# Optimization experiments

Measured on AMD Instinct MI355X. Metric: run time of the kernel, lower is better.

The kernel has to match this reference:

```python
import jax, jax.numpy as jnp
import numpy as np

B, N, E = 4, 1024, 8192
NF_IN, NF_H, NF_OUT = 32, 128, 3


def _lin(key, fan_in, fan_out):
    k1, k2 = jax.random.split(key)
    bound = 1.0 / np.sqrt(fan_in)
    W = jax.random.uniform(k1, (fan_in, fan_out), jnp.float32, -bound, bound)
    b = jax.random.uniform(k2, (fan_out,), jnp.float32, -bound, bound)
    return W, b


def setup_inputs() -> dict:
    key = jax.random.key(0)
    ks = jax.random.split(key, 16)
    x = jax.random.normal(ks[0], (B, N, NF_IN), jnp.float32)
    # One-hot receiver/sender relation matrices [B, E, N]
    recv = jax.random.randint(ks[1], (B, E), 0, N)
    send = jax.random.randint(ks[2], (B, E), 0, N)
    Rr = jax.nn.one_hot(recv, N, dtype=jnp.float32)
    Rs = jax.nn.one_hot(send, N, dtype=jnp.float32)
    neW0, neb0 = _lin(ks[3], NF_IN, NF_H)
    neW1, neb1 = _lin(ks[4], NF_H, NF_H)
    neW2, neb2 = _lin(ks[5], NF_H, NF_H)
    eeW0, eeb0 = _lin(ks[6], NF_IN * 2, NF_H)
    eeW1, eeb1 = _lin(ks[7], NF_H, NF_H)
    eeW2, eeb2 = _lin(ks[8], NF_H, NF_H)
    npW, npb = _lin(ks[9], NF_H * 2, NF_H)
    epW, epb = _lin(ks[10], NF_H * 3, NF_H)
    ppW0, ppb0 = _lin(ks[11], NF_H * 2, NF_H)
    ppW1, ppb1 = _lin(ks[12], NF_H, NF_H)
    ppW2, ppb2 = _lin(ks[13], NF_H, NF_OUT)
    return dict(x=x, Rr=Rr, Rs=Rs, pstep=2,
                neW0=neW0, neb0=neb0, neW1=neW1, neb1=neb1, neW2=neW2, neb2=neb2,
                eeW0=eeW0, eeb0=eeb0, eeW1=eeW1, eeb1=eeb1, eeW2=eeW2, eeb2=eeb2,
                npW=npW, npb=npb, epW=epW, epb=epb,
                ppW0=ppW0, ppb0=ppb0, ppW1=ppW1, ppb1=ppb1, ppW2=ppW2, ppb2=ppb2)


def _encoder(x, W0, b0, W1, b1, W2, b2):
    # Linear->ReLU x3 (ReLU after last layer too)
    h = jax.nn.relu(x @ W0 + b0)
    h = jax.nn.relu(h @ W1 + b1)
    return jax.nn.relu(h @ W2 + b2)


def _predictor(x, W0, b0, W1, b1, W2, b2):
    h = jax.nn.relu(x @ W0 + b0)
    h = jax.nn.relu(h @ W1 + b1)
    return h @ W2 + b2


def reference(x, Rr, Rs, pstep,
              neW0, neb0, neW1, neb1, neW2, neb2,
              eeW0, eeb0, eeW1, eeb1, eeW2, eeb2,
              npW, npb, epW, epb,
              ppW0, ppb0, ppW1, ppb1, ppW2, ppb2):
    node_encode = _encoder(x, neW0, neb0, neW1, neb1, neW2, neb2)  # [B,N,H]
    node_effect = node_encode
    x_r = jnp.einsum('ben,bnf->bef', Rr, x)  # gather receiver features
    x_s = jnp.einsum('ben,bnf->bef', Rs, x)  # gather sender features
    edge_encode = _encoder(jnp.concatenate([x_r, x_s], -1),
                           eeW0, eeb0, eeW1, eeb1, eeW2, eeb2)  # [B,E,H]
    for _ in range(pstep):
        ne_r = jnp.einsum('ben,bnh->beh', Rr, node_effect)
        ne_s = jnp.einsum('ben,bnh->beh', Rs, node_effect)
        edge_in = jnp.concatenate([edge_encode, ne_r, ne_s], -1)  # [B,E,3H]
        edge_effect = jax.nn.relu(edge_in @ epW + epb)  # [B,E,H]
        agg = jnp.einsum('ben,beh->bnh', Rr, edge_effect)  # scatter-add to receivers
        node_in = jnp.concatenate([node_encode, agg], -1)  # [B,N,2H]
        node_effect = jax.nn.relu(node_in @ npW + npb + node_effect)  # residual
    node_reps = _predictor(jnp.concatenate([node_encode, node_effect], -1),
                           ppW0, ppb0, ppW1, ppb1, ppW2, ppb2)  # [B,N,out]
    return node_reps
```

## Files before the change

### kernel.cpp

```cpp
#include <hip/hip_runtime.h>
#include <hip/hip_bf16.h>


typedef unsigned short u16;
typedef __attribute__((ext_vector_type(8))) __bf16 bf16x8;
typedef __attribute__((ext_vector_type(4))) float f32x4;

#define N_    1024
#define BN    4096
#define BE    32768
#define LOG_E 13
#define H_    128
#define LSTR  132
#define ECAP  64
#define ASTR  136

__device__ __forceinline__ u16 f2bf(float f) {
    __bf16 h = (__bf16)f;
    return __builtin_bit_cast(u16, h);
}

__device__ __forceinline__ bf16x8 cvt8(float4 f0, float4 f1) {
    bf16x8 a;
    a[0] = (__bf16)f0.x; a[1] = (__bf16)f0.y; a[2] = (__bf16)f0.z; a[3] = (__bf16)f0.w;
    a[4] = (__bf16)f1.x; a[5] = (__bf16)f1.y; a[6] = (__bf16)f1.z; a[7] = (__bf16)f1.w;
    return a;
}

__device__ __forceinline__ bf16x8 a_from_f32(const float* p) {
    float4 f0 = *(const float4*)p;
    float4 f1 = *(const float4*)(p + 4);
    return cvt8(f0, f1);
}

__device__ __forceinline__ bf16x8 a_from_lds(const float* lds, int r, int quad, int c) {
    return a_from_f32(lds + r * LSTR + c * 32 + quad * 8);
}

__device__ __forceinline__ void mm8(const u16* __restrict__ Wf, int c, bf16x8 a,
                                    f32x4* acc, int lane) {
    const u16* wp = Wf + ((size_t)c * 8) * 64 * 8;
    #pragma unroll
    for (int nt = 0; nt < 8; ++nt) {
        bf16x8 bw = *(const bf16x8*)(wp + (size_t)(nt * 64 + lane) * 8);
        acc[nt] = __builtin_amdgcn_mfma_f32_16x16x32_bf16(a, bw, acc[nt], 0, 0, 0);
    }
}

__device__ __forceinline__ void mm4(const u16* __restrict__ Wf, int c, int ntb,
                                    bf16x8 a, f32x4* acc, int lane) {
    const u16* wp = Wf + ((size_t)c * 8) * 64 * 8;
    #pragma unroll
    for (int nt = 0; nt < 4; ++nt) {
        bf16x8 bw = *(const bf16x8*)(wp + (size_t)((ntb + nt) * 64 + lane) * 8);
        acc[nt] = __builtin_amdgcn_mfma_f32_16x16x32_bf16(a, bw, acc[nt], 0, 0, 0);
    }
}

__device__ __forceinline__ void mm2(const u16* __restrict__ Wf, int c, int ntb,
                                    bf16x8 a, f32x4* acc, int lane) {
    const u16* wp = Wf + ((size_t)c * 8) * 64 * 8;
    #pragma unroll
    for (int nt = 0; nt < 2; ++nt) {
        bf16x8 bw = *(const bf16x8*)(wp + (size_t)((ntb + nt) * 64 + lane) * 8);
        acc[nt] = __builtin_amdgcn_mfma_f32_16x16x32_bf16(a, bw, acc[nt], 0, 0, 0);
    }
}

__device__ __forceinline__ void zacc8(f32x4* acc) {
    #pragma unroll
    for (int t = 0; t < 8; ++t) acc[t] = (f32x4){0.f, 0.f, 0.f, 0.f};
}
__device__ __forceinline__ void zacc4(f32x4* acc) {
    #pragma unroll
    for (int t = 0; t < 4; ++t) acc[t] = (f32x4){0.f, 0.f, 0.f, 0.f};
}

__device__ __forceinline__ void epi8_lds(float* lds, const f32x4* acc,
                                         const float* __restrict__ bias,
                                         int quad, int m) {
    #pragma unroll
    for (int nt = 0; nt < 8; ++nt) {
        float bv = bias[nt * 16 + m];
        #pragma unroll
        for (int i = 0; i < 4; ++i)
            lds[(quad * 4 + i) * LSTR + nt * 16 + m] = fmaxf(acc[nt][i] + bv, 0.f);
    }
}

__device__ __forceinline__ void epi4_lds(float* lds, const f32x4* acc,
                                         const float* __restrict__ bias,
                                         int quad, int m, int ntb) {
    #pragma unroll
    for (int nt = 0; nt < 4; ++nt) {
        int col = (ntb + nt) * 16 + m;
        float bv = bias[col];
        #pragma unroll
        for (int i = 0; i < 4; ++i)
            lds[(quad * 4 + i) * LSTR + col] = fmaxf(acc[nt][i] + bv, 0.f);
    }
}

struct WDesc { const float* src; u16* dst; int K; };
struct WPack { WDesc d[10]; };

__global__ __launch_bounds__(256) void k_wprep(WPack P, int* __restrict__ deg) {
    if (blockIdx.y == 10) {
        int i = blockIdx.x * 256 + threadIdx.x;
        if (i < BN / 4) ((int4*)deg)[i] = make_int4(0, 0, 0, 0);
        return;
    }
    WDesc d = P.d[blockIdx.y];
    int i = blockIdx.x * 256 + threadIdx.x;
    if (i >= d.K * 128) return;
    int j    = i & 7;
    int lane = (i >> 3) & 63;
    int nt   = (i >> 9) & 7;
    int c    = i >> 12;
    int k = c * 32 + (lane >> 4) * 8 + j;
    int n = nt * 16 + (lane & 15);
    d.dst[i] = f2bf(d.src[k * 128 + n]);
}

__global__ __launch_bounds__(256) void k_extract(const float* __restrict__ Rr,
                                                 const float* __restrict__ Rs,
                                                 int* __restrict__ recv,
                                                 int* __restrict__ send,
                                                 int* __restrict__ deg,
                                                 int* __restrict__ eidx) {
    int wave = threadIdx.x >> 6, lane = threadIdx.x & 63;
    int g = blockIdx.x * 4 + wave;
    const float* src;
    int* dst;
    if (g < BE) { src = Rr + (size_t)g * N_;        dst = recv + g; }
    else        { src = Rs + (size_t)(g - BE) * N_; dst = send + (g - BE); }
    int idx = 0;
    bool done = false;
    #pragma unroll
    for (int it = 0; it < 4; ++it) {
        if (!done) {
            int base = it * 256 + lane * 4;
            float4 v = *(const float4*)(src + base);
            int found = -1;
            if      (v.x != 0.f) found = base;
            else if (v.y != 0.f) found = base + 1;
            else if (v.z != 0.f) found = base + 2;
            else if (v.w != 0.f) found = base + 3;
            unsigned long long msk = __ballot(found >= 0);
            if (msk) {
                int sl = __ffsll((long long)msk) - 1;
                idx = __shfl(found, sl, 64);
                done = true;
            }
        }
    }
    if (lane == 0) {
        *dst = idx;
        if (g < BE) {
            int node = (g >> LOG_E) * N_ + idx;
            int pos = atomicAdd(deg + node, 1);
            if (pos < ECAP) eidx[node * ECAP + pos] = g;
        }
    }
}

__global__ __launch_bounds__(128) void k_node3(
    const float* __restrict__ x,
    const u16* __restrict__ W0, const float* __restrict__ b0,
    const u16* __restrict__ W1, const float* __restrict__ b1,
    const u16* __restrict__ W2, const float* __restrict__ b2,
    float* __restrict__ nenc_f, u16* __restrict__ nenc_bf)
{
    __shared__ float lds[2][16 * LSTR];
    int tid = threadIdx.x, lane = tid & 63, w = tid >> 6;
    int m = lane & 15, quad = lane >> 4;
    int row16 = blockIdx.x * 16, ntb = w * 4;
    f32x4 acc[4];

    zacc4(acc);
    mm4(W0, 0, ntb, a_from_f32(x + (size_t)(row16 + m) * 32 + quad * 8), acc, lane);
    epi4_lds(lds[0], acc, b0, quad, m, ntb);
    __syncthreads();

    zacc4(acc);
    #pragma unroll
    for (int c = 0; c < 4; ++c) mm4(W1, c, ntb, a_from_lds(lds[0], m, quad, c), acc, lane);
    epi4_lds(lds[1], acc, b1, quad, m, ntb);
    __syncthreads();

    zacc4(acc);
    #pragma unroll
    for (int c = 0; c < 4; ++c) mm4(W2, c, ntb, a_from_lds(lds[1], m, quad, c), acc, lane);
    epi4_lds(lds[0], acc, b2, quad, m, ntb);
    __syncthreads();

    #pragma unroll
    for (int t = 0; t < 16; ++t) {
        int flat = t * 128 + tid, r = flat >> 7, col = flat & 127;
        nenc_f[(size_t)(row16 + r) * H_ + col] = lds[0][r * LSTR + col];
    }
    #pragma unroll
    for (int t = 0; t < 8; ++t) {
        int p = t * 128 + tid, r = p >> 6, c2 = (p & 63) * 2;
        u16 lo = f2bf(lds[0][r * LSTR + c2]);
        u16 hi = f2bf(lds[0][r * LSTR + c2 + 1]);
        *(unsigned*)(nenc_bf + (size_t)(row16 + r) * H_ + c2) =
            (unsigned)lo | ((unsigned)hi << 16);
    }
}

__global__ __launch_bounds__(64) void k_edge3(
    const float* __restrict__ x,
    const int* __restrict__ recv, const int* __restrict__ send,
    const u16* __restrict__ W0, const float* __restrict__ b0,
    const u16* __restrict__ W1, const float* __restrict__ b1,
    const u16* __restrict__ W2, const float* __restrict__ b2,
    u16* __restrict__ eenc)
{
    __shared__ float lds[2][16 * LSTR];
    int lane = threadIdx.x, m = lane & 15, quad = lane >> 4;
    int row16 = blockIdx.x * 16;
    int e = row16 + m, b = e >> LOG_E;
    long rr = (long)b * N_ + recv[e];
    long rs = (long)b * N_ + send[e];
    f32x4 acc[8];

    zacc8(acc);
    mm8(W0, 0, a_from_f32(x + rr * 32 + quad * 8), acc, lane);
    mm8(W0, 1, a_from_f32(x + rs * 32 + quad * 8), acc, lane);
    epi8_lds(lds[0], acc, b0, quad, m);

    zacc8(acc);
    #pragma unroll
    for (int c = 0; c < 4; ++c) mm8(W1, c, a_from_lds(lds[0], m, quad, c), acc, lane);
    epi8_lds(lds[1], acc, b1, quad, m);

    zacc8(acc);
    #pragma unroll
    for (int c = 0; c < 4; ++c) mm8(W2, c, a_from_lds(lds[1], m, quad, c), acc, lane);
    epi8_lds(lds[0], acc, b2, quad, m);

    #pragma unroll
    for (int t = 0; t < 16; ++t) {
        int col = lane * 2;
        u16 lo = f2bf(lds[0][t * LSTR + col]);
        u16 hi = f2bf(lds[0][t * LSTR + col + 1]);
        *(unsigned*)(eenc + (size_t)(row16 + t) * H_ + col) =
            (unsigned)lo | ((unsigned)hi << 16);
    }
}

__global__ __launch_bounds__(64) void k_eprop(
    const u16* __restrict__ eenc, const u16* __restrict__ eff_bf,
    const int* __restrict__ recv, const int* __restrict__ send,
    const u16* __restrict__ Wf, const float* __restrict__ bias,
    float* __restrict__ edge_eff)
{
    int lane = threadIdx.x, m = lane & 15, quad = lane >> 4;
    int row16 = blockIdx.x * 16;
    int e = row16 + m;
    long rr = ((long)(e >> LOG_E) * N_ + recv[e]) * H_;
    long rs = ((long)(e >> LOG_E) * N_ + send[e]) * H_;
    f32x4 acc[8];
    zacc8(acc);

    #pragma unroll
    for (int c = 0; c < 4; ++c)
        mm8(Wf, c, *(const bf16x8*)(eenc + (size_t)e * H_ + c * 32 + quad * 8), acc, lane);
    #pragma unroll
    for (int c = 0; c < 4; ++c)
        mm8(Wf, 4 + c, *(const bf16x8*)(eff_bf + rr + c * 32 + quad * 8), acc, lane);
    #pragma unroll
    for (int c = 0; c < 4; ++c)
        mm8(Wf, 8 + c, *(const bf16x8*)(eff_bf + rs + c * 32 + quad * 8), acc, lane);

    #pragma unroll
    for (int nt = 0; nt < 8; ++nt) {
        int col = nt * 16 + m;
        float bv = bias[col];
        #pragma unroll
        for (int i = 0; i < 4; ++i)
            edge_eff[(size_t)(row16 + quad * 4 + i) * H_ + col] =
                fmaxf(acc[nt][i] + bv, 0.f);
    }
}

__global__ __launch_bounds__(256) void k_nprop(
    const u16* __restrict__ nenc_bf, const float* __restrict__ edge_eff,
    const int* __restrict__ deg, const int* __restrict__ eidx,
    const float* __restrict__ eff_f,
    const u16* __restrict__ Wf, const float* __restrict__ bias,
    float* __restrict__ nout_f, u16* __restrict__ nout_bf)
{
    __shared__ u16 aggl[16 * ASTR];
    int tid = threadIdx.x, lane = tid & 63, w = tid >> 6;
    int m = lane & 15, quad = lane >> 4;
    int row16 = blockIdx.x * 16;

    int nd = tid >> 4, l = tid & 15;
    int node = row16 + nd;
    int dg = deg[node]; dg = dg < ECAP ? dg : ECAP;
    int ev = eidx[node * ECAP + l];
    int base = lane & 48;
    float s[8] = {0.f, 0.f, 0.f, 0.f, 0.f, 0.f, 0.f, 0.f};
    int d16 = dg < 16 ? dg : 16;
    int t = 0;
    for (; t + 1 < d16; t += 2) {
        int e0 = __shfl(ev, base | t, 64);
        int e1 = __shfl(ev, base | (t + 1), 64);
        const float* p0 = edge_eff + (size_t)e0 * H_ + l * 8;
        const float* p1 = edge_eff + (size_t)e1 * H_ + l * 8;
        float4 a0 = *(const float4*)p0, b0 = *(const float4*)(p0 + 4);
        float4 a1 = *(const float4*)p1, b1 = *(const float4*)(p1 + 4);
        s[0] += a0.x + a1.x; s[1] += a0.y + a1.y;
        s[2] += a0.z + a1.z; s[3] += a0.w + a1.w;
        s[4] += b0.x + b1.x; s[5] += b0.y + b1.y;
        s[6] += b0.z + b1.z; s[7] += b0.w + b1.w;
    }
    if (t < d16) {
        int e0 = __shfl(ev, base | t, 64);
        const float* p0 = edge_eff + (size_t)e0 * H_ + l * 8;
        float4 a0 = *(const float4*)p0, b0 = *(const float4*)(p0 + 4);
        s[0] += a0.x; s[1] += a0.y; s[2] += a0.z; s[3] += a0.w;
        s[4] += b0.x; s[5] += b0.y; s[6] += b0.z; s[7] += b0.w;
        ++t;
    }
    for (; t < dg; ++t) {
        int e0 = eidx[node * ECAP + t];
        const float* p0 = edge_eff + (size_t)e0 * H_ + l * 8;
        float4 a0 = *(const float4*)p0, b0 = *(const float4*)(p0 + 4);
        s[0] += a0.x; s[1] += a0.y; s[2] += a0.z; s[3] += a0.w;
        s[4] += b0.x; s[5] += b0.y; s[6] += b0.z; s[7] += b0.w;
    }
    bf16x8 o;
    #pragma unroll
    for (int j = 0; j < 8; ++j) o[j] = (__bf16)s[j];
    *(bf16x8*)(aggl + nd * ASTR + l * 8) = o;
    __syncthreads();

    int row = row16 + m, ntb = w * 2;
    f32x4 acc[2];
    acc[0] = (f32x4){0.f, 0.f, 0.f, 0.f};
    acc[1] = (f32x4){0.f, 0.f, 0.f, 0.f};

    #pragma unroll
    for (int c = 0; c < 4; ++c)
        mm2(Wf, c, ntb,
            *(const bf16x8*)(nenc_bf + (size_t)row * H_ + c * 32 + quad * 8), acc, lane);
    #pragma unroll
    for (int c = 0; c < 4; ++c)
        mm2(Wf, 4 + c, ntb,
            *(const bf16x8*)(aggl + m * ASTR + c * 32 + quad * 8), acc, lane);

    #pragma unroll
    for (int nt = 0; nt < 2; ++nt) {
        int col = (ntb + nt) * 16 + m;
        float bv = bias[col];
        #pragma unroll
        for (int i = 0; i < 4; ++i) {
            int r = row16 + quad * 4 + i;
            float v = fmaxf(acc[nt][i] + bv + eff_f[(size_t)r * H_ + col], 0.f);
            nout_f[(size_t)r * H_ + col] = v;
            nout_bf[(size_t)r * H_ + col] = f2bf(v);
        }
    }
}

__global__ __launch_bounds__(128) void k_pred(
    const u16* __restrict__ nenc_bf, const u16* __restrict__ eff_bf,
    const u16* __restrict__ W0, const float* __restrict__ b0,
    const u16* __restrict__ W1, const float* __restrict__ b1,
    const float* __restrict__ W2, const float* __restrict__ b2,
    float* __restrict__ out)
{
    __shared__ float lds[2][16 * LSTR];
    int tid = threadIdx.x, lane = tid & 63, w = tid >> 6;
    int m = lane & 15, quad = lane >> 4;
    int row16 = blockIdx.x * 16, row = row16 + m, ntb = w * 4;
    f32x4 acc[4];

    zacc4(acc);
    #pragma unroll
    for (int c = 0; c < 4; ++c)
        mm4(W0, c, ntb,
            *(const bf16x8*)(nenc_bf + (size_t)row * H_ + c * 32 + quad * 8), acc, lane);
    #pragma unroll
    for (int c = 0; c < 4; ++c)
        mm4(W0, 4 + c, ntb,
            *(const bf16x8*)(eff_bf + (size_t)row * H_ + c * 32 + quad * 8), acc, lane);
    epi4_lds(lds[0], acc, b0, quad, m, ntb);
    __syncthreads();

    zacc4(acc);
    #pragma unroll
    for (int c = 0; c < 4; ++c) mm4(W1, c, ntb, a_from_lds(lds[0], m, quad, c), acc, lane);
    epi4_lds(lds[1], acc, b1, quad, m, ntb);
    __syncthreads();

    if (w == 0) {
        int r = lane & 15, col = lane >> 4;
        if (col < 3) {
            float s = 0.f;
            #pragma unroll 8
            for (int k = 0; k < 128; ++k)
                s += lds[1][r * LSTR + k] * W2[k * 3 + col];
            out[(size_t)(row16 + r) * 3 + col] = s + b2[col];
        }
    }
}

extern "C" void kernel_launch(void* const* d_in, const int* in_sizes, int n_in,
                              void* d_out, int out_size, void* d_ws, size_t ws_size,
                              hipStream_t stream) {
    (void)in_sizes; (void)n_in; (void)out_size; (void)ws_size;

    const float* x    = (const float*)d_in[0];
    const float* Rr   = (const float*)d_in[1];
    const float* Rs   = (const float*)d_in[2];
    const float* neW0 = (const float*)d_in[4];  const float* neb0 = (const float*)d_in[5];
    const float* neW1 = (const float*)d_in[6];  const float* neb1 = (const float*)d_in[7];
    const float* neW2 = (const float*)d_in[8];  const float* neb2 = (const float*)d_in[9];
    const float* eeW0 = (const float*)d_in[10]; const float* eeb0 = (const float*)d_in[11];
    const float* eeW1 = (const float*)d_in[12]; const float* eeb1 = (const float*)d_in[13];
    const float* eeW2 = (const float*)d_in[14]; const float* eeb2 = (const float*)d_in[15];
    const float* npW  = (const float*)d_in[16]; const float* npb  = (const float*)d_in[17];
    const float* epW  = (const float*)d_in[18]; const float* epb  = (const float*)d_in[19];
    const float* ppW0 = (const float*)d_in[20]; const float* ppb0 = (const float*)d_in[21];
    const float* ppW1 = (const float*)d_in[22]; const float* ppb1 = (const float*)d_in[23];
    const float* ppW2 = (const float*)d_in[24]; const float* ppb2 = (const float*)d_in[25];

    char* ws = (char*)d_ws;
    size_t off = 0;
    auto alloc = [&](size_t bytes) -> char* {
        char* p = ws + off;
        off += (bytes + 255) & ~(size_t)255;
        return p;
    };

    u16* f_neW0 = (u16*)alloc(32  * 128 * 2);
    u16* f_neW1 = (u16*)alloc(128 * 128 * 2);
    u16* f_neW2 = (u16*)alloc(128 * 128 * 2);
    u16* f_eeW0 = (u16*)alloc(64  * 128 * 2);
    u16* f_eeW1 = (u16*)alloc(128 * 128 * 2);
    u16* f_eeW2 = (u16*)alloc(128 * 128 * 2);
    u16* f_epW  = (u16*)alloc(384 * 128 * 2);
    u16* f_npW  = (u16*)alloc(256 * 128 * 2);
    u16* f_ppW0 = (u16*)alloc(256 * 128 * 2);
    u16* f_ppW1 = (u16*)alloc(128 * 128 * 2);
    int*   recv = (int*)alloc(BE * 4);
    int*   send = (int*)alloc(BE * 4);
    int*   deg  = (int*)alloc(BN * 4);
    int*   eidx = (int*)alloc((size_t)BN * ECAP * 4);
    float* nenc_f  = (float*)alloc((size_t)BN * H_ * 4);
    u16*   nenc_bf = (u16*)alloc((size_t)BN * H_ * 2);
    float* nef1_f  = (float*)alloc((size_t)BN * H_ * 4);
    u16*   nef1_bf = (u16*)alloc((size_t)BN * H_ * 2);
    float* nef2_f  = (float*)alloc((size_t)BN * H_ * 4);
    u16*   nef2_bf = (u16*)alloc((size_t)BN * H_ * 2);
    float* edge_eff = (float*)alloc((size_t)BE * H_ * 4);
    u16*   eenc = (u16*)alloc((size_t)BE * H_ * 2);

    WPack P;
    P.d[0] = {neW0, f_neW0, 32};
    P.d[1] = {neW1, f_neW1, 128};
    P.d[2] = {neW2, f_neW2, 128};
    P.d[3] = {eeW0, f_eeW0, 64};
    P.d[4] = {eeW1, f_eeW1, 128};
    P.d[5] = {eeW2, f_eeW2, 128};
    P.d[6] = {epW,  f_epW,  384};
    P.d[7] = {npW,  f_npW,  256};
    P.d[8] = {ppW0, f_ppW0, 256};
    P.d[9] = {ppW1, f_ppW1, 128};
    k_wprep<<<dim3(192, 11), 256, 0, stream>>>(P, deg);

    k_extract<<<(2 * BE) / 4, 256, 0, stream>>>(Rr, Rs, recv, send, deg, eidx);

    k_node3<<<BN / 16, 128, 0, stream>>>(x, f_neW0, neb0, f_neW1, neb1, f_neW2, neb2,
                                         nenc_f, nenc_bf);
    k_edge3<<<BE / 16, 64, 0, stream>>>(x, recv, send,
                                        f_eeW0, eeb0, f_eeW1, eeb1, f_eeW2, eeb2, eenc);

    k_eprop<<<BE / 16, 64, 0, stream>>>(eenc, nenc_bf, recv, send, f_epW, epb, edge_eff);
    k_nprop<<<BN / 16, 256, 0, stream>>>(nenc_bf, edge_eff, deg, eidx, nenc_f,
                                         f_npW, npb, nef1_f, nef1_bf);
    k_eprop<<<BE / 16, 64, 0, stream>>>(eenc, nef1_bf, recv, send, f_epW, epb, edge_eff);
    k_nprop<<<BN / 16, 256, 0, stream>>>(nenc_bf, edge_eff, deg, eidx, nef1_f,
                                         f_npW, npb, nef2_f, nef2_bf);

    k_pred<<<BN / 16, 128, 0, stream>>>(nenc_bf, nef2_bf, f_ppW0, ppb0, f_ppW1, ppb1,
                                        ppW2, ppb2, (float*)d_out);
}
```

Measured before the change: 375.5 us.

## Merge prep, encoder and final propagation+predictor kernels; split eprop across two waves

Merges weight prep and one-hot index extraction into a single launch, with the degree counters zeroed by a memset. Node and edge encoders become one launch using 128-thread blocks. The last node-propagation step is fused with the predictor MLP, so that step's node effects stay in LDS and are never written to global memory. Edge propagation now splits the output columns across two waves per block, which doubles the wave count but makes each wave load half the weights. The aim is fewer launches, less global traffic and better occupancy, at the cost of larger fused kernels.

```diff
diff --git a/kernel.cpp b/kernel.cpp
--- a/kernel.cpp
+++ b/kernel.cpp
@@ -37,16 +37,6 @@
     return a_from_f32(lds + r * LSTR + c * 32 + quad * 8);
 }
 
-__device__ __forceinline__ void mm8(const u16* __restrict__ Wf, int c, bf16x8 a,
-                                    f32x4* acc, int lane) {
-    const u16* wp = Wf + ((size_t)c * 8) * 64 * 8;
-    #pragma unroll
-    for (int nt = 0; nt < 8; ++nt) {
-        bf16x8 bw = *(const bf16x8*)(wp + (size_t)(nt * 64 + lane) * 8);
-        acc[nt] = __builtin_amdgcn_mfma_f32_16x16x32_bf16(a, bw, acc[nt], 0, 0, 0);
-    }
-}
-
 __device__ __forceinline__ void mm4(const u16* __restrict__ Wf, int c, int ntb,
                                     bf16x8 a, f32x4* acc, int lane) {
     const u16* wp = Wf + ((size_t)c * 8) * 64 * 8;
@@ -67,25 +57,13 @@
     }
 }
 
-__device__ __forceinline__ void zacc8(f32x4* acc) {
-    #pragma unroll
-    for (int t = 0; t < 8; ++t) acc[t] = (f32x4){0.f, 0.f, 0.f, 0.f};
-}
 __device__ __forceinline__ void zacc4(f32x4* acc) {
     #pragma unroll
     for (int t = 0; t < 4; ++t) acc[t] = (f32x4){0.f, 0.f, 0.f, 0.f};
 }
-
-__device__ __forceinline__ void epi8_lds(float* lds, const f32x4* acc,
-                                         const float* __restrict__ bias,
-                                         int quad, int m) {
-    #pragma unroll
-    for (int nt = 0; nt < 8; ++nt) {
-        float bv = bias[nt * 16 + m];
-        #pragma unroll
-        for (int i = 0; i < 4; ++i)
-            lds[(quad * 4 + i) * LSTR + nt * 16 + m] = fmaxf(acc[nt][i] + bv, 0.f);
-    }
+__device__ __forceinline__ void zacc2(f32x4* acc) {
+    acc[0] = (f32x4){0.f, 0.f, 0.f, 0.f};
+    acc[1] = (f32x4){0.f, 0.f, 0.f, 0.f};
 }
 
 __device__ __forceinline__ void epi4_lds(float* lds, const f32x4* acc,
@@ -104,32 +82,30 @@
 struct WDesc { const float* src; u16* dst; int K; };
 struct WPack { WDesc d[10]; };
 
-__global__ __launch_bounds__(256) void k_wprep(WPack P, int* __restrict__ deg) {
-    if (blockIdx.y == 10) {
-        int i = blockIdx.x * 256 + threadIdx.x;
-        if (i < BN / 4) ((int4*)deg)[i] = make_int4(0, 0, 0, 0);
+__global__ __launch_bounds__(256) void k_prep(WPack P,
+                                              const float* __restrict__ Rr,
+                                              const float* __restrict__ Rs,
+                                              int* __restrict__ recv,
+                                              int* __restrict__ send,
+                                              int* __restrict__ deg,
+                                              int* __restrict__ eidx) {
+    int bx = blockIdx.x;
+    if (bx >= 16384) {
+        int t = bx - 16384;
+        WDesc d = P.d[t / 192];
+        int i = (t % 192) * 256 + threadIdx.x;
+        if (i >= d.K * 128) return;
+        int j    = i & 7;
+        int lane = (i >> 3) & 63;
+        int nt   = (i >> 9) & 7;
+        int c    = i >> 12;
+        int k = c * 32 + (lane >> 4) * 8 + j;
+        int n = nt * 16 + (lane & 15);
+        d.dst[i] = f2bf(d.src[k * 128 + n]);
         return;
     }
-    WDesc d = P.d[blockIdx.y];
-    int i = blockIdx.x * 256 + threadIdx.x;
-    if (i >= d.K * 128) return;
-    int j    = i & 7;
-    int lane = (i >> 3) & 63;
-    int nt   = (i >> 9) & 7;
-    int c    = i >> 12;
-    int k = c * 32 + (lane >> 4) * 8 + j;
-    int n = nt * 16 + (lane & 15);
-    d.dst[i] = f2bf(d.src[k * 128 + n]);
-}
-
-__global__ __launch_bounds__(256) void k_extract(const float* __restrict__ Rr,
-                                                 const float* __restrict__ Rs,
-                                                 int* __restrict__ recv,
-                                                 int* __restrict__ send,
-                                                 int* __restrict__ deg,
-                                                 int* __restrict__ eidx) {
     int wave = threadIdx.x >> 6, lane = threadIdx.x & 63;
-    int g = blockIdx.x * 4 + wave;
+    int g = bx * 4 + wave;
     const float* src;
     int* dst;
     if (g < BE) { src = Rr + (size_t)g * N_;        dst = recv + g; }
@@ -164,119 +140,127 @@
     }
 }
 
-__global__ __launch_bounds__(128) void k_node3(
+__global__ __launch_bounds__(128) void k_enc(
     const float* __restrict__ x,
-    const u16* __restrict__ W0, const float* __restrict__ b0,
-    const u16* __restrict__ W1, const float* __restrict__ b1,
-    const u16* __restrict__ W2, const float* __restrict__ b2,
-    float* __restrict__ nenc_f, u16* __restrict__ nenc_bf)
+    const int* __restrict__ recv, const int* __restrict__ send,
+    const u16* __restrict__ nW0, const float* __restrict__ nb0,
+    const u16* __restrict__ nW1, const float* __restrict__ nb1,
+    const u16* __restrict__ nW2, const float* __restrict__ nb2,
+    const u16* __restrict__ eW0, const float* __restrict__ eb0,
+    const u16* __restrict__ eW1, const float* __restrict__ eb1,
+    const u16* __restrict__ eW2, const float* __restrict__ eb2,
+    float* __restrict__ nenc_f, u16* __restrict__ nenc_bf,
+    u16* __restrict__ eenc)
 {
     __shared__ float lds[2][16 * LSTR];
     int tid = threadIdx.x, lane = tid & 63, w = tid >> 6;
     int m = lane & 15, quad = lane >> 4;
-    int row16 = blockIdx.x * 16, ntb = w * 4;
+    int ntb = w * 4;
     f32x4 acc[4];
 
+    if (blockIdx.x < 256) {
+        int row16 = blockIdx.x * 16;
+        zacc4(acc);
+        mm4(nW0, 0, ntb, a_from_f32(x + (size_t)(row16 + m) * 32 + quad * 8), acc, lane);
+        epi4_lds(lds[0], acc, nb0, quad, m, ntb);
+        __syncthreads();
+
+        zacc4(acc);
+        #pragma unroll
+        for (int c = 0; c < 4; ++c)
+            mm4(nW1, c, ntb, a_from_lds(lds[0], m, quad, c), acc, lane);
+        epi4_lds(lds[1], acc, nb1, quad, m, ntb);
+        __syncthreads();
+
+        zacc4(acc);
+        #pragma unroll
+        for (int c = 0; c < 4; ++c)
+            mm4(nW2, c, ntb, a_from_lds(lds[1], m, quad, c), acc, lane);
+        epi4_lds(lds[0], acc, nb2, quad, m, ntb);
+        __syncthreads();
+
+        #pragma unroll
+        for (int t = 0; t < 16; ++t) {
+            int flat = t * 128 + tid, r = flat >> 7, col = flat & 127;
+            nenc_f[(size_t)(row16 + r) * H_ + col] = lds[0][r * LSTR + col];
+        }
+        #pragma unroll
+        for (int t = 0; t < 8; ++t) {
+            int p = t * 128 + tid, r = p >> 6, c2 = (p & 63) * 2;
+            u16 lo = f2bf(lds[0][r * LSTR + c2]);
+            u16 hi = f2bf(lds[0][r * LSTR + c2 + 1]);
+            *(unsigned*)(nenc_bf + (size_t)(row16 + r) * H_ + c2) =
+                (unsigned)lo | ((unsigned)hi << 16);
+        }
+        return;
+    }
+
+    int row16 = (blockIdx.x - 256) * 16;
+    int e = row16 + m, b = e >> LOG_E;
+    long rr = (long)b * N_ + recv[e];
+    long rs = (long)b * N_ + send[e];
+
     zacc4(acc);
-    mm4(W0, 0, ntb, a_from_f32(x + (size_t)(row16 + m) * 32 + quad * 8), acc, lane);
-    epi4_lds(lds[0], acc, b0, quad, m, ntb);
+    mm4(eW0, 0, ntb, a_from_f32(x + rr * 32 + quad * 8), acc, lane);
+    mm4(eW0, 1, ntb, a_from_f32(x + rs * 32 + quad * 8), acc, lane);
+    epi4_lds(lds[0], acc, eb0, quad, m, ntb);
     __syncthreads();
 
     zacc4(acc);
     #pragma unroll
-    for (int c = 0; c < 4; ++c) mm4(W1, c, ntb, a_from_lds(lds[0], m, quad, c), acc, lane);
-    epi4_lds(lds[1], acc, b1, quad, m, ntb);
+    for (int c = 0; c < 4; ++c)
+        mm4(eW1, c, ntb, a_from_lds(lds[0], m, quad, c), acc, lane);
+    epi4_lds(lds[1], acc, eb1, quad, m, ntb);
     __syncthreads();
 
     zacc4(acc);
     #pragma unroll
-    for (int c = 0; c < 4; ++c) mm4(W2, c, ntb, a_from_lds(lds[1], m, quad, c), acc, lane);
-    epi4_lds(lds[0], acc, b2, quad, m, ntb);
-    __syncthreads();
-
-    #pragma unroll
-    for (int t = 0; t < 16; ++t) {
-        int flat = t * 128 + tid, r = flat >> 7, col = flat & 127;
-        nenc_f[(size_t)(row16 + r) * H_ + col] = lds[0][r * LSTR + col];
-    }
+    for (int c = 0; c < 4; ++c)
+        mm4(eW2, c, ntb, a_from_lds(lds[1], m, quad, c), acc, lane);
+    epi4_lds(lds[0], acc, eb2, quad, m, ntb);
+    __syncthreads();
+
     #pragma unroll
     for (int t = 0; t < 8; ++t) {
         int p = t * 128 + tid, r = p >> 6, c2 = (p & 63) * 2;
         u16 lo = f2bf(lds[0][r * LSTR + c2]);
         u16 hi = f2bf(lds[0][r * LSTR + c2 + 1]);
-        *(unsigned*)(nenc_bf + (size_t)(row16 + r) * H_ + c2) =
+        *(unsigned*)(eenc + (size_t)(row16 + r) * H_ + c2) =
             (unsigned)lo | ((unsigned)hi << 16);
     }
 }
 
-__global__ __launch_bounds__(64) void k_edge3(
-    const float* __restrict__ x,
-    const int* __restrict__ recv, const int* __restrict__ send,
-    const u16* __restrict__ W0, const float* __restrict__ b0,
-    const u16* __restrict__ W1, const float* __restrict__ b1,
-    const u16* __restrict__ W2, const float* __restrict__ b2,
-    u16* __restrict__ eenc)
-{
-    __shared__ float lds[2][16 * LSTR];
-    int lane = threadIdx.x, m = lane & 15, quad = lane >> 4;
-    int row16 = blockIdx.x * 16;
-    int e = row16 + m, b = e >> LOG_E;
-    long rr = (long)b * N_ + recv[e];
-    long rs = (long)b * N_ + send[e];
-    f32x4 acc[8];
-
-    zacc8(acc);
-    mm8(W0, 0, a_from_f32(x + rr * 32 + quad * 8), acc, lane);
-    mm8(W0, 1, a_from_f32(x + rs * 32 + quad * 8), acc, lane);
-    epi8_lds(lds[0], acc, b0, quad, m);
-
-    zacc8(acc);
-    #pragma unroll
-    for (int c = 0; c < 4; ++c) mm8(W1, c, a_from_lds(lds[0], m, quad, c), acc, lane);
-    epi8_lds(lds[1], acc, b1, quad, m);
-
-    zacc8(acc);
-    #pragma unroll
-    for (int c = 0; c < 4; ++c) mm8(W2, c, a_from_lds(lds[1], m, quad, c), acc, lane);
-    epi8_lds(lds[0], acc, b2, quad, m);
-
-    #pragma unroll
-    for (int t = 0; t < 16; ++t) {
-        int col = lane * 2;
-        u16 lo = f2bf(lds[0][t * LSTR + col]);
-        u16 hi = f2bf(lds[0][t * LSTR + col + 1]);
-        *(unsigned*)(eenc + (size_t)(row16 + t) * H_ + col) =
-            (unsigned)lo | ((unsigned)hi << 16);
-    }
-}
-
-__global__ __launch_bounds__(64) void k_eprop(
+__global__ __launch_bounds__(128) void k_eprop(
     const u16* __restrict__ eenc, const u16* __restrict__ eff_bf,
     const int* __restrict__ recv, const int* __restrict__ send,
     const u16* __restrict__ Wf, const float* __restrict__ bias,
     float* __restrict__ edge_eff)
 {
-    int lane = threadIdx.x, m = lane & 15, quad = lane >> 4;
-    int row16 = blockIdx.x * 16;
+    int tid = threadIdx.x, lane = tid & 63, w = tid >> 6;
+    int m = lane & 15, quad = lane >> 4;
+    int row16 = blockIdx.x * 16, ntb = w * 4;
     int e = row16 + m;
     long rr = ((long)(e >> LOG_E) * N_ + recv[e]) * H_;
     long rs = ((long)(e >> LOG_E) * N_ + send[e]) * H_;
-    f32x4 acc[8];
-    zacc8(acc);
-
-    #pragma unroll
-    for (int c = 0; c < 4; ++c)
-        mm8(Wf, c, *(const bf16x8*)(eenc + (size_t)e * H_ + c * 32 + quad * 8), acc, lane);
-    #pragma unroll
-    for (int c = 0; c < 4; ++c)
-        mm8(Wf, 4 + c, *(const bf16x8*)(eff_bf + rr + c * 32 + quad * 8), acc, lane);
-    #pragma unroll
-    for (int c = 0; c < 4; ++c)
-        mm8(Wf, 8 + c, *(const bf16x8*)(eff_bf + rs + c * 32 + quad * 8), acc, lane);
-
-    #pragma unroll
-    for (int nt = 0; nt < 8; ++nt) {
-        int col = nt * 16 + m;
+    f32x4 acc[4];
+    zacc4(acc);
+
+    #pragma unroll
+    for (int c = 0; c < 4; ++c)
+        mm4(Wf, c, ntb,
+            *(const bf16x8*)(eenc + (size_t)e * H_ + c * 32 + quad * 8), acc, lane);
+    #pragma unroll
+    for (int c = 0; c < 4; ++c)
+        mm4(Wf, 4 + c, ntb,
+            *(const bf16x8*)(eff_bf + rr + c * 32 + quad * 8), acc, lane);
+    #pragma unroll
+    for (int c = 0; c < 4; ++c)
+        mm4(Wf, 8 + c, ntb,
+            *(const bf16x8*)(eff_bf + rs + c * 32 + quad * 8), acc, lane);
+
+    #pragma unroll
+    for (int nt = 0; nt < 4; ++nt) {
+        int col = (ntb + nt) * 16 + m;
         float bv = bias[col];
         #pragma unroll
         for (int i = 0; i < 4; ++i)
@@ -285,18 +269,10 @@
     }
 }
 
-__global__ __launch_bounds__(256) void k_nprop(
-    const u16* __restrict__ nenc_bf, const float* __restrict__ edge_eff,
-    const int* __restrict__ deg, const int* __restrict__ eidx,
-    const float* __restrict__ eff_f,
-    const u16* __restrict__ Wf, const float* __restrict__ bias,
-    float* __restrict__ nout_f, u16* __restrict__ nout_bf)
-{
-    __shared__ u16 aggl[16 * ASTR];
-    int tid = threadIdx.x, lane = tid & 63, w = tid >> 6;
-    int m = lane & 15, quad = lane >> 4;
-    int row16 = blockIdx.x * 16;
-
+__device__ __forceinline__ void gather_agg(u16* aggl, int row16, int tid, int lane,
+                                           const float* __restrict__ edge_eff,
+                                           const int* __restrict__ deg,
+                                           const int* __restrict__ eidx) {
     int nd = tid >> 4, l = tid & 15;
     int node = row16 + nd;
     int dg = deg[node]; dg = dg < ECAP ? dg : ECAP;
@@ -336,13 +312,26 @@
     #pragma unroll
     for (int j = 0; j < 8; ++j) o[j] = (__bf16)s[j];
     *(bf16x8*)(aggl + nd * ASTR + l * 8) = o;
+}
+
+__global__ __launch_bounds__(256) void k_nprop(
+    const u16* __restrict__ nenc_bf, const float* __restrict__ edge_eff,
+    const int* __restrict__ deg, const int* __restrict__ eidx,
+    const float* __restrict__ eff_f,
+    const u16* __restrict__ Wf, const float* __restrict__ bias,
+    float* __restrict__ nout_f, u16* __restrict__ nout_bf)
+{
+    __shared__ u16 aggl[16 * ASTR];
+    int tid = threadIdx.x, lane = tid & 63, w = tid >> 6;
+    int m = lane & 15, quad = lane >> 4;
+    int row16 = blockIdx.x * 16;
+
+    gather_agg(aggl, row16, tid, lane, edge_eff, deg, eidx);
     __syncthreads();
 
     int row = row16 + m, ntb = w * 2;
     f32x4 acc[2];
-    acc[0] = (f32x4){0.f, 0.f, 0.f, 0.f};
-    acc[1] = (f32x4){0.f, 0.f, 0.f, 0.f};
-
+    zacc2(acc);
     #pragma unroll
     for (int c = 0; c < 4; ++c)
         mm2(Wf, c, ntb,
@@ -366,35 +355,84 @@
     }
 }
 
-__global__ __launch_bounds__(128) void k_pred(
-    const u16* __restrict__ nenc_bf, const u16* __restrict__ eff_bf,
-    const u16* __restrict__ W0, const float* __restrict__ b0,
-    const u16* __restrict__ W1, const float* __restrict__ b1,
+__global__ __launch_bounds__(256) void k_npropred(
+    const u16* __restrict__ nenc_bf, const float* __restrict__ edge_eff,
+    const int* __restrict__ deg, const int* __restrict__ eidx,
+    const float* __restrict__ eff_f,
+    const u16* __restrict__ Wnp, const float* __restrict__ bnp,
+    const u16* __restrict__ Wp0, const float* __restrict__ bp0,
+    const u16* __restrict__ Wp1, const float* __restrict__ bp1,
     const float* __restrict__ W2, const float* __restrict__ b2,
     float* __restrict__ out)
 {
-    __shared__ float lds[2][16 * LSTR];
+    __shared__ u16 aggl[16 * ASTR];
+    __shared__ u16 vl[16 * ASTR];
+    __shared__ u16 h1[16 * ASTR];
+    __shared__ float h2[16 * LSTR];
     int tid = threadIdx.x, lane = tid & 63, w = tid >> 6;
     int m = lane & 15, quad = lane >> 4;
-    int row16 = blockIdx.x * 16, row = row16 + m, ntb = w * 4;
-    f32x4 acc[4];
-
-    zacc4(acc);
-    #pragma unroll
-    for (int c = 0; c < 4; ++c)
-        mm4(W0, c, ntb,
+    int row16 = blockIdx.x * 16;
+
+    gather_agg(aggl, row16, tid, lane, edge_eff, deg, eidx);
+    __syncthreads();
+
+    int row = row16 + m, ntb = w * 2;
+    f32x4 acc[2];
+
+    zacc2(acc);
+    #pragma unroll
+    for (int c = 0; c < 4; ++c)
+        mm2(Wnp, c, ntb,
             *(const bf16x8*)(nenc_bf + (size_t)row * H_ + c * 32 + quad * 8), acc, lane);
     #pragma unroll
     for (int c = 0; c < 4; ++c)
-        mm4(W0, 4 + c, ntb,
-            *(const bf16x8*)(eff_bf + (size_t)row * H_ + c * 32 + quad * 8), acc, lane);
-    epi4_lds(lds[0], acc, b0, quad, m, ntb);
-    __syncthreads();
-
-    zacc4(acc);
-    #pragma unroll
-    for (int c = 0; c < 4; ++c) mm4(W1, c, ntb, a_from_lds(lds[0], m, quad, c), acc, lane);
-    epi4_lds(lds[1], acc, b1, quad, m, ntb);
+        mm2(Wnp, 4 + c, ntb,
+            *(const bf16x8*)(aggl + m * ASTR + c * 32 + quad * 8), acc, lane);
+    #pragma unroll
+    for (int nt = 0; nt < 2; ++nt) {
+        int col = (ntb + nt) * 16 + m;
+        float bv = bnp[col];
+        #pragma unroll
+        for (int i = 0; i < 4; ++i) {
+            int r = quad * 4 + i;
+            float v = fmaxf(acc[nt][i] + bv + eff_f[(size_t)(row16 + r) * H_ + col], 0.f);
+            vl[r * ASTR + col] = f2bf(v);
+        }
+    }
+    __syncthreads();
+
+    zacc2(acc);
+    #pragma unroll
+    for (int c = 0; c < 4; ++c)
+        mm2(Wp0, c, ntb,
+            *(const bf16x8*)(nenc_bf + (size_t)row * H_ + c * 32 + quad * 8), acc, lane);
+    #pragma unroll
+    for (int c = 0; c < 4; ++c)
+        mm2(Wp0, 4 + c, ntb,
+            *(const bf16x8*)(vl + m * ASTR + c * 32 + quad * 8), acc, lane);
+    #pragma unroll
+    for (int nt = 0; nt < 2; ++nt) {
+        int col = (ntb + nt) * 16 + m;
+        float bv = bp0[col];
+        #pragma unroll
+        for (int i = 0; i < 4; ++i)
+            h1[(quad * 4 + i) * ASTR + col] = f2bf(fmaxf(acc[nt][i] + bv, 0.f));
+    }
+    __syncthreads();
+
+    zacc2(acc);
+    #pragma unroll
+    for (int c = 0; c < 4; ++c)
+        mm2(Wp1, c, ntb,
+            *(const bf16x8*)(h1 + m * ASTR + c * 32 + quad * 8), acc, lane);
+    #pragma unroll
+    for (int nt = 0; nt < 2; ++nt) {
+        int col = (ntb + nt) * 16 + m;
+        float bv = bp1[col];
+        #pragma unroll
+        for (int i = 0; i < 4; ++i)
+            h2[(quad * 4 + i) * LSTR + col] = fmaxf(acc[nt][i] + bv, 0.f);
+    }
     __syncthreads();
 
     if (w == 0) {
@@ -403,7 +441,7 @@
             float s = 0.f;
             #pragma unroll 8
             for (int k = 0; k < 128; ++k)
-                s += lds[1][r * LSTR + k] * W2[k * 3 + col];
+                s += h2[r * LSTR + k] * W2[k * 3 + col];
             out[(size_t)(row16 + r) * 3 + col] = s + b2[col];
         }
     }
@@ -455,8 +493,6 @@
     u16*   nenc_bf = (u16*)alloc((size_t)BN * H_ * 2);
     float* nef1_f  = (float*)alloc((size_t)BN * H_ * 4);
     u16*   nef1_bf = (u16*)alloc((size_t)BN * H_ * 2);
-    float* nef2_f  = (float*)alloc((size_t)BN * H_ * 4);
-    u16*   nef2_bf = (u16*)alloc((size_t)BN * H_ * 2);
     float* edge_eff = (float*)alloc((size_t)BE * H_ * 4);
     u16*   eenc = (u16*)alloc((size_t)BE * H_ * 2);
 
@@ -471,22 +507,21 @@
     P.d[7] = {npW,  f_npW,  256};
     P.d[8] = {ppW0, f_ppW0, 256};
     P.d[9] = {ppW1, f_ppW1, 128};
-    k_wprep<<<dim3(192, 11), 256, 0, stream>>>(P, deg);
-
-    k_extract<<<(2 * BE) / 4, 256, 0, stream>>>(Rr, Rs, recv, send, deg, eidx);
-
-    k_node3<<<BN / 16, 128, 0, stream>>>(x, f_neW0, neb0, f_neW1, neb1, f_neW2, neb2,
-                                         nenc_f, nenc_bf);
-    k_edge3<<<BE / 16, 64, 0, stream>>>(x, recv, send,
-                                        f_eeW0, eeb0, f_eeW1, eeb1, f_eeW2, eeb2, eenc);
-
-    k_eprop<<<BE / 16, 64, 0, stream>>>(eenc, nenc_bf, recv, send, f_epW, epb, edge_eff);
+
+    hipMemsetAsync(deg, 0, BN * 4, stream);
+
+    k_prep<<<16384 + 1920, 256, 0, stream>>>(P, Rr, Rs, recv, send, deg, eidx);
+
+    k_enc<<<256 + 2048, 128, 0, stream>>>(x, recv, send,
+                                          f_neW0, neb0, f_neW1, neb1, f_neW2, neb2,
+                                          f_eeW0, eeb0, f_eeW1, eeb1, f_eeW2, eeb2,
+                                          nenc_f, nenc_bf, eenc);
+
+    k_eprop<<<BE / 16, 128, 0, stream>>>(eenc, nenc_bf, recv, send, f_epW, epb, edge_eff);
     k_nprop<<<BN / 16, 256, 0, stream>>>(nenc_bf, edge_eff, deg, eidx, nenc_f,
                                          f_npW, npb, nef1_f, nef1_bf);
-    k_eprop<<<BE / 16, 64, 0, stream>>>(eenc, nef1_bf, recv, send, f_epW, epb, edge_eff);
-    k_nprop<<<BN / 16, 256, 0, stream>>>(nenc_bf, edge_eff, deg, eidx, nef1_f,
-                                         f_npW, npb, nef2_f, nef2_bf);
-
-    k_pred<<<BN / 16, 128, 0, stream>>>(nenc_bf, nef2_bf, f_ppW0, ppb0, f_ppW1, ppb1,
-                                        ppW2, ppb2, (float*)d_out);
-}
+    k_eprop<<<BE / 16, 128, 0, stream>>>(eenc, nef1_bf, recv, send, f_epW, epb, edge_eff);
+    k_npropred<<<BN / 16, 256, 0, stream>>>(nenc_bf, edge_eff, deg, eidx, nef1_f,
+                                            f_npW, npb, f_ppW0, ppb0, f_ppW1, ppb1,
+                                            ppW2, ppb2, (float*)d_out);
+}
```

Result: no change. 370.4 us (-1.4%).
